# Kernel tuning notes

Measured on AMD Instinct MI355X. Metric: run time of the kernel, lower is better.

## Reference

```python
import jax, jax.numpy as jnp
import numpy as np

N_NODES = 100000
N_EDGES = 1600000
D_IN, D_HID, D_OUT = 128, 128, 40


def _sgconv(feat, W, b, src, dst, n_nodes):
    # DGL SGConv, k=1, norm='both': D^{-1/2} A D^{-1/2} X W + b
    ones = jnp.ones(dst.shape, dtype=feat.dtype)
    deg = jax.ops.segment_sum(ones, dst, num_segments=n_nodes)  # in-degrees
    norm = jnp.clip(deg, 1.0) ** -0.5  # [N]
    h = feat * norm[:, None]
    # sparse aggregation: gather from src, scatter-add to dst
    h = jax.ops.segment_sum(h[src], dst, num_segments=n_nodes)  # [N, d]
    h = h * norm[:, None]
    return h @ W + b


def setup_inputs() -> dict:
    key = jax.random.key(0)
    ks = jax.random.split(key, 6)
    features = jax.random.normal(ks[0], (N_NODES, D_IN), dtype=jnp.float32)
    src = jax.random.randint(ks[1], (N_EDGES,), 0, N_NODES, dtype=jnp.int32)
    dst = jax.random.randint(ks[2], (N_EDGES,), 0, N_NODES, dtype=jnp.int32)
    # Xavier-uniform init like DGL's fc
    lim1 = float(np.sqrt(6.0 / (D_IN + D_HID)))
    lim2 = float(np.sqrt(6.0 / (D_HID + D_OUT)))
    W1 = jax.random.uniform(ks[3], (D_IN, D_HID), jnp.float32, -lim1, lim1)
    b1 = jnp.zeros((D_HID,), dtype=jnp.float32)
    W2 = jax.random.uniform(ks[4], (D_HID, D_OUT), jnp.float32, -lim2, lim2)
    b2 = jnp.zeros((D_OUT,), dtype=jnp.float32)
    return {"features": features, "src": src, "dst": dst,
            "W1": W1, "b1": b1, "W2": W2, "b2": b2, "n_nodes": N_NODES}


def reference(features, src, dst, W1, b1, W2, b2, n_nodes):
    x = _sgconv(features, W1, b1, src, dst, n_nodes)
    x = jax.nn.elu(x)
    x = _sgconv(x, W2, b2, src, dst, n_nodes)
    return x
```

## Files before the change

kernel.cpp:

```cpp
#include <hip/hip_runtime.h>
#include <hip/hip_fp16.h>
#include <math.h>


#define DIN  128
#define DHID 128
#define DOUT 40
#define BSHIFT 9
#define BNODES 512

union U8  { uint2 u; __half2 h[2]; };
union U16 { uint4 u; __half2 h[4]; };

typedef _Float16     f16x8 __attribute__((ext_vector_type(8)));
typedef float        f32x4 __attribute__((ext_vector_type(4)));
union F16X8 { uint4 u; f16x8 f; };
union HCV   { __half h; unsigned short s; };
union FV4   { float4 h; f32x4 v; };

__device__ __forceinline__ float elu_f(float x) {
    return x > 0.0f ? x : (expf(x) - 1.0f);
}

__global__ void prep_pass1(const float* __restrict__ W1, const float* __restrict__ W2,
                           __half* __restrict__ w1f, __half* __restrict__ w2f,
                           const int* __restrict__ src, const int* __restrict__ dst,
                           int E, int NB, int cap,
                           int* __restrict__ bcur, int* __restrict__ bbuf) {
    __shared__ int cnt[256];
    __shared__ int wcur[256];
    if (blockIdx.x < 11) {
        int tid = blockIdx.x * 256 + threadIdx.x;
        if (tid < 2048) {
            int l = tid & 63;
            int t = (tid >> 6) & 3;
            int c = tid >> 8;
            int kb = t * 32 + (l >> 4) * 8, col = c * 16 + (l & 15);
            #pragma unroll
            for (int j = 0; j < 8; ++j)
                w1f[tid * 8 + j] = __float2half_rn(W1[(kb + j) * DHID + col]);
        } else if (tid < 2048 + 768) {
            int id = tid - 2048;
            int l = id & 63;
            int t = (id >> 6) & 3;
            int c = id >> 8;
            int kb = t * 32 + (l >> 4) * 8, col = c * 16 + (l & 15);
            #pragma unroll
            for (int j = 0; j < 8; ++j)
                w2f[id * 8 + j] = (col < DOUT) ? __float2half_rn(W2[(kb + j) * DOUT + col])
                                               : __float2half_rn(0.f);
        }
        return;
    }
    int bid = blockIdx.x - 11;
    int nblk = gridDim.x - 11;
    const int CHUNK = 8192;
    for (long base = (long)bid * CHUNK; base < E; base += (long)nblk * CHUNK) {
        int n = min(CHUNK, (int)(E - base));
        if (threadIdx.x < 256) cnt[threadIdx.x] = 0;
        __syncthreads();
        for (int i = threadIdx.x; i < n; i += blockDim.x) {
            int b = dst[base + i] >> BSHIFT;
            atomicAdd(&cnt[b], 1);
        }
        __syncthreads();
        if (threadIdx.x < NB) {
            int c = cnt[threadIdx.x];
            wcur[threadIdx.x] = (c > 0) ? atomicAdd(&bcur[threadIdx.x], c) : 0;
        }
        __syncthreads();
        for (int i = threadIdx.x; i < n; i += blockDim.x) {
            int s = src[base + i];
            int d = dst[base + i];
            int b = d >> BSHIFT;
            int slot = atomicAdd(&wcur[b], 1);
            if (slot < cap) bbuf[(long)b * cap + slot] = (s << BSHIFT) | (d & (BNODES - 1));
        }
        __syncthreads();
    }
}

__global__ void pass2_sort(const int* __restrict__ bbuf, const int* __restrict__ bcur,
                           int N, int NB, int cap,
                           float* __restrict__ norm, int* __restrict__ rowptr,
                           int* __restrict__ esrc) {
    __shared__ int cnt[BNODES];
    __shared__ int scnt[256];
    __shared__ int sgbase;
    int tid = threadIdx.x;
    int b = blockIdx.x;
    scnt[tid] = (tid < NB) ? bcur[tid] : 0;
    __syncthreads();
    if (tid == 0) {
        int run = 0;
        for (int i = 0; i < NB; ++i) { if (i == b) sgbase = run; run += scnt[i]; }
        if (b == NB - 1) rowptr[N] = run;
    }
    __syncthreads();
    int gbase = sgbase;
    int n_b = min(bcur[b], cap);
    int dbase = b << BSHIFT;
    const int* eb = bbuf + (long)b * cap;
    for (int i = tid; i < BNODES; i += blockDim.x) cnt[i] = 0;
    __syncthreads();
    for (int i = tid; i < n_b; i += blockDim.x)
        atomicAdd(&cnt[eb[i] & (BNODES - 1)], 1);
    __syncthreads();
    for (int i = tid; i < BNODES; i += blockDim.x) {
        int d = dbase + i;
        if (d < N) norm[d] = rsqrtf(fmaxf((float)cnt[i], 1.0f));
    }
    __syncthreads();
    if (tid == 0) {
        int run = 0;
        #pragma unroll 4
        for (int i = 0; i < BNODES; ++i) { int c = cnt[i]; cnt[i] = run; run += c; }
    }
    __syncthreads();
    for (int i = tid; i < BNODES; i += blockDim.x) {
        int d = dbase + i;
        if (d < N) rowptr[d] = gbase + cnt[i];
    }
    __syncthreads();
    for (int i = tid; i < n_b; i += blockDim.x) {
        int v = eb[i];
        int slot = atomicAdd(&cnt[v & (BNODES - 1)], 1);
        esrc[gbase + slot] = ((unsigned)v) >> BSHIFT;
    }
}

__global__ void perm_yconv(const int* __restrict__ rowptr, int* __restrict__ perm,
                           const float* __restrict__ feat, const float* __restrict__ norm,
                           __half* __restrict__ y, int N, int npermblk) {
    __shared__ int lcnt[1024];
    __shared__ int lbase[1024];
    if ((int)blockIdx.x < npermblk) {
        const int CHUNK = 4096;
        for (long base = (long)blockIdx.x * CHUNK; base < N; base += (long)npermblk * CHUNK) {
            int n = min(CHUNK, (int)(N - base));
            for (int i = threadIdx.x; i < 1024; i += 256) lcnt[i] = 0;
            __syncthreads();
            for (int i = threadIdx.x; i < n; i += 256) {
                int d = min(rowptr[base + i + 1] - rowptr[base + i], 1023);
                atomicAdd(&lcnt[d], 1);
            }
            __syncthreads();
            if (threadIdx.x == 0) {
                int run = 0;
                for (int i = 0; i < 1024; ++i) { int c = lcnt[i]; lbase[i] = run; run += c; }
            }
            __syncthreads();
            for (int i = threadIdx.x; i < 1024; i += 256) lcnt[i] = 0;
            __syncthreads();
            for (int i = threadIdx.x; i < n; i += 256) {
                int d = min(rowptr[base + i + 1] - rowptr[base + i], 1023);
                int pos = lbase[d] + atomicAdd(&lcnt[d], 1);
                perm[base + pos] = base + (int)i;
            }
            __syncthreads();
        }
        return;
    }
    long total = (long)N * 32;
    long stride = (long)(gridDim.x - npermblk) * 256;
    const float4* f4 = reinterpret_cast<const float4*>(feat);
    uint2* y2 = reinterpret_cast<uint2*>(y);
    for (long i = (long)(blockIdx.x - npermblk) * 256 + threadIdx.x; i < total; i += stride) {
        int n = (int)(i >> 5);
        float nm = norm[n];
        float4 v = f4[i];
        U8 o;
        o.h[0] = __floats2half2_rn(v.x * nm, v.y * nm);
        o.h[1] = __floats2half2_rn(v.z * nm, v.w * nm);
        y2[i] = o.u;
    }
}

__global__ void norm_from_deg(const int* __restrict__ deg, float* __restrict__ norm, int N) {
    int stride = gridDim.x * blockDim.x;
    for (int i = blockIdx.x * blockDim.x + threadIdx.x; i < N; i += stride)
        norm[i] = rsqrtf(fmaxf((float)deg[i], 1.0f));
}

__global__ void degi_kernel(const int* __restrict__ dst, int E, int* __restrict__ deg) {
    int stride = gridDim.x * blockDim.x;
    for (int i = blockIdx.x * blockDim.x + threadIdx.x; i < E; i += stride)
        atomicAdd(&deg[dst[i]], 1);
}


__global__ void gather1_kernel(const __half* __restrict__ y, const int* __restrict__ rowptr,
                               const int* __restrict__ esrc, const int* __restrict__ perm,
                               const float* __restrict__ norm,
                               __half* __restrict__ aggh, int N) {
    int lane = threadIdx.x & 15;
    long g = ((long)blockIdx.x * blockDim.x + threadIdx.x) >> 4;
    long gstride = ((long)gridDim.x * blockDim.x) >> 4;
    const uint4* y4 = reinterpret_cast<const uint4*>(y);
    uint4* a4 = reinterpret_cast<uint4*>(aggh);
    for (long gi = g; gi < N; gi += gstride) {
        int n = perm[gi];
        int beg = rowptr[n], end = rowptr[n + 1];
        float a0 = 0.f, a1 = 0.f, a2 = 0.f, a3 = 0.f;
        float a4f = 0.f, a5 = 0.f, a6 = 0.f, a7 = 0.f;
        int j = beg;
        for (; j + 1 < end; j += 2) {
            int s0 = esrc[j], s1 = esrc[j + 1];
            U16 u0, u1;
            u0.u = y4[(long)s0 * 16 + lane];
            u1.u = y4[(long)s1 * 16 + lane];
            float2 p0 = __half22float2(u0.h[0]), p1 = __half22float2(u0.h[1]);
            float2 p2 = __half22float2(u0.h[2]), p3 = __half22float2(u0.h[3]);
            float2 q0 = __half22float2(u1.h[0]), q1 = __half22float2(u1.h[1]);
            float2 q2 = __half22float2(u1.h[2]), q3 = __half22float2(u1.h[3]);
            a0 += p0.x + q0.x; a1 += p0.y + q0.y;
            a2 += p1.x + q1.x; a3 += p1.y + q1.y;
            a4f += p2.x + q2.x; a5 += p2.y + q2.y;
            a6 += p3.x + q3.x; a7 += p3.y + q3.y;
        }
        if (j < end) {
            int s0 = esrc[j];
            U16 u0; u0.u = y4[(long)s0 * 16 + lane];
            float2 p0 = __half22float2(u0.h[0]), p1 = __half22float2(u0.h[1]);
            float2 p2 = __half22float2(u0.h[2]), p3 = __half22float2(u0.h[3]);
            a0 += p0.x; a1 += p0.y; a2 += p1.x; a3 += p1.y;
            a4f += p2.x; a5 += p2.y; a6 += p3.x; a7 += p3.y;
        }
        float nm = norm[n];
        U16 o;
        o.h[0] = __floats2half2_rn(a0 * nm, a1 * nm);
        o.h[1] = __floats2half2_rn(a2 * nm, a3 * nm);
        o.h[2] = __floats2half2_rn(a4f * nm, a5 * nm);
        o.h[3] = __floats2half2_rn(a6 * nm, a7 * nm);
        a4[(long)n * 16 + lane] = o.u;
    }
}

__global__ void gather2_kernel(const __half* __restrict__ z, const int* __restrict__ rowptr,
                               const int* __restrict__ esrc, const int* __restrict__ perm,
                               const float* __restrict__ norm, const float* __restrict__ b2,
                               float* __restrict__ out, int N) {
    int lane = threadIdx.x & 63;
    int grp = lane / 5;
    int seg = lane - grp * 5;
    bool act = grp < 12;
    long wglob = ((long)blockIdx.x * blockDim.x + threadIdx.x) >> 6;
    long g0 = wglob * 12 + grp;
    long gstride = (((long)gridDim.x * blockDim.x) >> 6) * 12;
    const uint4* z4 = reinterpret_cast<const uint4*>(z);
    for (long gi = g0; gi < N; gi += gstride) {
        if (act) {
            int n = perm[gi];
            int beg = rowptr[n], end = rowptr[n + 1];
            float a0 = 0.f, a1 = 0.f, a2 = 0.f, a3 = 0.f;
            float a4f = 0.f, a5 = 0.f, a6 = 0.f, a7 = 0.f;
            int j = beg;
            for (; j + 1 < end; j += 2) {
                int s0 = esrc[j], s1 = esrc[j + 1];
                U16 u0, u1;
                u0.u = z4[(long)s0 * 5 + seg];
                u1.u = z4[(long)s1 * 5 + seg];
                float2 p0 = __half22float2(u0.h[0]), p1 = __half22float2(u0.h[1]);
                float2 p2 = __half22float2(u0.h[2]), p3 = __half22float2(u0.h[3]);
                float2 q0 = __half22float2(u1.h[0]), q1 = __half22float2(u1.h[1]);
                float2 q2 = __half22float2(u1.h[2]), q3 = __half22float2(u1.h[3]);
                a0 += p0.x + q0.x; a1 += p0.y + q0.y;
                a2 += p1.x + q1.x; a3 += p1.y + q1.y;
                a4f += p2.x + q2.x; a5 += p2.y + q2.y;
                a6 += p3.x + q3.x; a7 += p3.y + q3.y;
            }
            if (j < end) {
                int s0 = esrc[j];
                U16 u0; u0.u = z4[(long)s0 * 5 + seg];
                float2 p0 = __half22float2(u0.h[0]), p1 = __half22float2(u0.h[1]);
                float2 p2 = __half22float2(u0.h[2]), p3 = __half22float2(u0.h[3]);
                a0 += p0.x; a1 += p0.y; a2 += p1.x; a3 += p1.y;
                a4f += p2.x; a5 += p2.y; a6 += p3.x; a7 += p3.y;
            }
            float nm = norm[n];
            const float4* b4 = reinterpret_cast<const float4*>(b2);
            float4 bb0 = b4[seg * 2], bb1 = b4[seg * 2 + 1];
            FV4 o0, o1;
            o0.h.x = fmaf(a0, nm, bb0.x); o0.h.y = fmaf(a1, nm, bb0.y);
            o0.h.z = fmaf(a2, nm, bb0.z); o0.h.w = fmaf(a3, nm, bb0.w);
            o1.h.x = fmaf(a4f, nm, bb1.x); o1.h.y = fmaf(a5, nm, bb1.y);
            o1.h.z = fmaf(a6, nm, bb1.z); o1.h.w = fmaf(a7, nm, bb1.w);
            f32x4* out4 = reinterpret_cast<f32x4*>(out);
            __builtin_nontemporal_store(o0.v, &out4[(long)n * 10 + seg * 2]);
            __builtin_nontemporal_store(o1.v, &out4[(long)n * 10 + seg * 2 + 1]);
        }
    }
}


__launch_bounds__(256, 2)
__global__ void mmfused_kernel(const __half* __restrict__ aggh,
                               const __half* __restrict__ w1f, const __half* __restrict__ w2f,
                               const float* __restrict__ b1, const float* __restrict__ norm,
                               __half* __restrict__ z, int N) {
    __shared__ uint4 w1l[2048];
    __shared__ uint4 w2l[768];
    __shared__ unsigned short hl[64 * 128];
    int tid = threadIdx.x;
    const uint4* w1g = reinterpret_cast<const uint4*>(w1f);
    const uint4* w2g = reinterpret_cast<const uint4*>(w2f);
    for (int i = tid; i < 2048; i += 256) w1l[i] = w1g[i];
    for (int i = tid; i < 768; i += 256) w2l[i] = w2g[i];
    __syncthreads();

    int w = tid >> 6, l = tid & 63;
    int lr = l & 15, lg = l >> 4;
    float b1v[8];
    #pragma unroll
    for (int c = 0; c < 8; ++c) b1v[c] = b1[c * 16 + lr];

    int ntiles = (N + 63) >> 6;
    const uint4* ag = reinterpret_cast<const uint4*>(aggh);
    for (int tile = blockIdx.x; tile < ntiles; tile += gridDim.x) {
        int rb = tile << 6;
        int arow = rb + w * 16 + lr;
        int arc = min(arow, N - 1);
        F16X8 af[4];
        #pragma unroll
        for (int t = 0; t < 4; ++t) af[t].u = ag[(long)arc * 16 + t * 4 + lg];
        #pragma unroll
        for (int c = 0; c < 8; ++c) {
            f32x4 acc = {b1v[c], b1v[c], b1v[c], b1v[c]};
            #pragma unroll
            for (int t = 0; t < 4; ++t) {
                F16X8 bf; bf.u = w1l[(c * 4 + t) * 64 + l];
                acc = __builtin_amdgcn_mfma_f32_16x16x32_f16(af[t].f, bf.f, acc, 0, 0, 0);
            }
            int colb2 = (c * 16 + lr) * 2;
            #pragma unroll
            for (int i = 0; i < 4; ++i) {
                int rl = w * 16 + lg * 4 + i;
                HCV cv; cv.h = __float2half_rn(elu_f(acc[i]));
                int ba = (rl * 256 + colb2) ^ ((rl & 7) << 4);
                *reinterpret_cast<unsigned short*>(reinterpret_cast<char*>(hl) + ba) = cv.s;
            }
        }
        int rl2 = w * 16 + lr;
        int sw = (rl2 & 7) << 4;
        F16X8 hf[4];
        #pragma unroll
        for (int t = 0; t < 4; ++t) {
            int ba = (rl2 * 256 + (t * 32 + lg * 8) * 2) ^ sw;
            hf[t].u = *reinterpret_cast<const uint4*>(reinterpret_cast<const char*>(hl) + ba);
        }
        float nmv[4];
        #pragma unroll
        for (int i = 0; i < 4; ++i) {
            int r = rb + w * 16 + lg * 4 + i;
            nmv[i] = norm[min(r, N - 1)];
        }
        #pragma unroll
        for (int c = 0; c < 3; ++c) {
            f32x4 acc = {0.f, 0.f, 0.f, 0.f};
            #pragma unroll
            for (int t = 0; t < 4; ++t) {
                F16X8 bf; bf.u = w2l[(c * 4 + t) * 64 + l];
                acc = __builtin_amdgcn_mfma_f32_16x16x32_f16(hf[t].f, bf.f, acc, 0, 0, 0);
            }
            int col = c * 16 + lr;
            if (col < DOUT) {
                #pragma unroll
                for (int i = 0; i < 4; ++i) {
                    int r = rb + w * 16 + lg * 4 + i;
                    if (r < N) z[(long)r * DOUT + col] = __float2half_rn(acc[i] * nmv[i]);
                }
            }
        }
    }
}


__global__ void scatter1_kernel(const float* __restrict__ feat, const int* __restrict__ src,
                                const int* __restrict__ dst, const float* __restrict__ norm,
                                float* __restrict__ agg, int E) {
    long T = (long)blockIdx.x * blockDim.x + threadIdx.x;
    int l4 = (int)(T & 31);
    long e = T >> 5;
    long estride = ((long)gridDim.x * blockDim.x) >> 5;
    for (; e < E; e += estride) {
        int s = src[e], d = dst[e];
        float ns = norm[s];
        float4 v = reinterpret_cast<const float4*>(feat)[(long)s * 32 + l4];
        float* o = agg + (long)d * DIN + l4 * 4;
        atomicAdd(o + 0, v.x * ns);
        atomicAdd(o + 1, v.y * ns);
        atomicAdd(o + 2, v.z * ns);
        atomicAdd(o + 3, v.w * ns);
    }
}

__global__ void scatter2_kernel(const float* __restrict__ z, const int* __restrict__ src,
                                const int* __restrict__ dst, float* __restrict__ out, int E) {
    long T = (long)blockIdx.x * blockDim.x + threadIdx.x;
    int l = (int)(T & 15);
    long e = T >> 4;
    long estride = ((long)gridDim.x * blockDim.x) >> 4;
    for (; e < E; e += estride) {
        if (l < 10) {
            int s = src[e], d = dst[e];
            float4 v = reinterpret_cast<const float4*>(z)[(long)s * 10 + l];
            float* o = out + (long)d * DOUT + l * 4;
            atomicAdd(o + 0, v.x);
            atomicAdd(o + 1, v.y);
            atomicAdd(o + 2, v.z);
            atomicAdd(o + 3, v.w);
        }
    }
}

__launch_bounds__(256, 2)
__global__ void mm1f_kernel(float* __restrict__ xh, const float* __restrict__ W1,
                            const float* __restrict__ b1, const float* __restrict__ norm,
                            int N) {
    __shared__ float Wl[DIN * DHID];
    __shared__ float Xl[32 * DIN];
    for (int i = threadIdx.x; i < DIN * DHID; i += 256) Wl[i] = W1[i];
    int cg = threadIdx.x & 31;
    int rg = threadIdx.x >> 5;
    int c0 = cg * 4;
    for (long r0 = (long)blockIdx.x * 32; r0 < N; r0 += (long)gridDim.x * 32) {
        __syncthreads();
        for (int i = threadIdx.x; i < 32 * 32; i += 256) {
            int rr = i >> 5;
            long row = r0 + rr;
            float4 v = make_float4(0.f, 0.f, 0.f, 0.f);
            if (row < N) {
                v = reinterpret_cast<const float4*>(xh)[row * 32 + (i & 31)];
                float nm = norm[row];
                v.x *= nm; v.y *= nm; v.z *= nm; v.w *= nm;
            }
            reinterpret_cast<float4*>(Xl)[i] = v;
        }
        __syncthreads();
        float acc[4][4];
        float bx = b1[c0], by = b1[c0 + 1], bz = b1[c0 + 2], bw = b1[c0 + 3];
        #pragma unroll
        for (int r = 0; r < 4; ++r) { acc[r][0] = bx; acc[r][1] = by; acc[r][2] = bz; acc[r][3] = bw; }
        for (int k = 0; k < DIN; k += 4) {
            float4 w0 = *reinterpret_cast<const float4*>(&Wl[(k + 0) * DHID + c0]);
            float4 w1 = *reinterpret_cast<const float4*>(&Wl[(k + 1) * DHID + c0]);
            float4 w2 = *reinterpret_cast<const float4*>(&Wl[(k + 2) * DHID + c0]);
            float4 w3 = *reinterpret_cast<const float4*>(&Wl[(k + 3) * DHID + c0]);
            #pragma unroll
            for (int r = 0; r < 4; ++r) {
                float4 x = *reinterpret_cast<const float4*>(&Xl[(rg * 4 + r) * DIN + k]);
                acc[r][0] = fmaf(x.x, w0.x, fmaf(x.y, w1.x, fmaf(x.z, w2.x, fmaf(x.w, w3.x, acc[r][0]))));
                acc[r][1] = fmaf(x.x, w0.y, fmaf(x.y, w1.y, fmaf(x.z, w2.y, fmaf(x.w, w3.y, acc[r][1]))));
                acc[r][2] = fmaf(x.x, w0.z, fmaf(x.y, w1.z, fmaf(x.z, w2.z, fmaf(x.w, w3.z, acc[r][2]))));
                acc[r][3] = fmaf(x.x, w0.w, fmaf(x.y, w1.w, fmaf(x.z, w2.w, fmaf(x.w, w3.w, acc[r][3]))));
            }
        }
        #pragma unroll
        for (int r = 0; r < 4; ++r) {
            long row = r0 + rg * 4 + r;
            if (row < N) {
                float4 o;
                o.x = elu_f(acc[r][0]); o.y = elu_f(acc[r][1]);
                o.z = elu_f(acc[r][2]); o.w = elu_f(acc[r][3]);
                *reinterpret_cast<float4*>(&xh[row * DIN + c0]) = o;
            }
        }
    }
}

__launch_bounds__(256, 2)
__global__ void mm2f_kernel(const float* __restrict__ h, const float* __restrict__ W2,
                            const float* __restrict__ norm, float* __restrict__ z, int N) {
    __shared__ float Wl[DHID * DOUT];
    __shared__ float Xl[64 * DIN];
    for (int i = threadIdx.x; i < DHID * DOUT; i += 256) Wl[i] = W2[i];
    int cg = threadIdx.x & 15;
    int rg = threadIdx.x >> 4;
    int c0 = cg * 4;
    for (long r0 = (long)blockIdx.x * 64; r0 < N; r0 += (long)gridDim.x * 64) {
        __syncthreads();
        for (int i = threadIdx.x; i < 64 * 32; i += 256) {
            int rr = i >> 5;
            long row = r0 + rr;
            float4 v = make_float4(0.f, 0.f, 0.f, 0.f);
            if (row < N) v = reinterpret_cast<const float4*>(h)[row * 32 + (i & 31)];
            reinterpret_cast<float4*>(Xl)[i] = v;
        }
        __syncthreads();
        if (c0 < DOUT) {
            float acc[4][4];
            #pragma unroll
            for (int r = 0; r < 4; ++r) { acc[r][0] = 0.f; acc[r][1] = 0.f; acc[r][2] = 0.f; acc[r][3] = 0.f; }
            for (int k = 0; k < DHID; k += 4) {
                float4 w0 = *reinterpret_cast<const float4*>(&Wl[(k + 0) * DOUT + c0]);
                float4 w1 = *reinterpret_cast<const float4*>(&Wl[(k + 1) * DOUT + c0]);
                float4 w2 = *reinterpret_cast<const float4*>(&Wl[(k + 2) * DOUT + c0]);
                float4 w3 = *reinterpret_cast<const float4*>(&Wl[(k + 3) * DOUT + c0]);
                #pragma unroll
                for (int r = 0; r < 4; ++r) {
                    float4 x = *reinterpret_cast<const float4*>(&Xl[(rg * 4 + r) * DIN + k]);
                    acc[r][0] = fmaf(x.x, w0.x, fmaf(x.y, w1.x, fmaf(x.z, w2.x, fmaf(x.w, w3.x, acc[r][0]))));
                    acc[r][1] = fmaf(x.x, w0.y, fmaf(x.y, w1.y, fmaf(x.z, w2.y, fmaf(x.w, w3.y, acc[r][1]))));
                    acc[r][2] = fmaf(x.x, w0.z, fmaf(x.y, w1.z, fmaf(x.z, w2.z, fmaf(x.w, w3.z, acc[r][2]))));
                    acc[r][3] = fmaf(x.x, w0.w, fmaf(x.y, w1.w, fmaf(x.z, w2.w, fmaf(x.w, w3.w, acc[r][3]))));
                }
            }
            #pragma unroll
            for (int r = 0; r < 4; ++r) {
                long row = r0 + rg * 4 + r;
                if (row < N) {
                    float nm = norm[row];
                    float4 o;
                    o.x = acc[r][0] * nm; o.y = acc[r][1] * nm;
                    o.z = acc[r][2] * nm; o.w = acc[r][3] * nm;
                    *reinterpret_cast<float4*>(&z[row * DOUT + c0]) = o;
                }
            }
        }
    }
}

__global__ void final_kernel(float* __restrict__ out, const float* __restrict__ norm,
                             const float* __restrict__ b2, int N) {
    long total = (long)N * DOUT;
    long stride = (long)gridDim.x * blockDim.x;
    for (long i = (long)blockIdx.x * blockDim.x + threadIdx.x; i < total; i += stride) {
        int n = (int)(i / DOUT), d = (int)(i % DOUT);
        out[i] = fmaf(out[i], norm[n], b2[d]);
    }
}


static inline size_t al4k(size_t x) { return (x + 4095) & ~(size_t)4095; }

extern "C" void kernel_launch(void* const* d_in, const int* in_sizes, int n_in,
                              void* d_out, int out_size, void* d_ws, size_t ws_size,
                              hipStream_t stream) {
    const float* feat = (const float*)d_in[0];
    const int*   src  = (const int*)d_in[1];
    const int*   dst  = (const int*)d_in[2];
    const float* W1   = (const float*)d_in[3];
    const float* b1   = (const float*)d_in[4];
    const float* W2   = (const float*)d_in[5];
    const float* b2   = (const float*)d_in[6];
    int N = in_sizes[0] / DIN;
    int E = in_sizes[1];
    float* out = (float*)d_out;
    char* ws = (char*)d_ws;

    int NB = (N + BNODES - 1) >> BSHIFT;
    int cap = ((E / (NB > 0 ? NB : 1)) * 5 / 4 + 256 + 1) & ~1;

    size_t o_norm   = 0;
    size_t o_rowptr = o_norm   + al4k((size_t)N * 4);
    size_t o_bcur   = o_rowptr + al4k(((size_t)N + 1) * 4);
    size_t o_perm   = o_bcur   + al4k((size_t)(NB + 1) * 4);
    size_t o_esrc   = o_perm   + al4k((size_t)N * 4);
    size_t o_aggh   = o_esrc   + al4k((size_t)E * 4);
    size_t o_y      = o_aggh   + al4k((size_t)N * DIN * 2);
    size_t o_z      = o_y      + al4k((size_t)N * DIN * 2);
    size_t o_w1f    = o_z      + al4k((size_t)N * DOUT * 2);
    size_t o_w2f    = o_w1f    + al4k((size_t)16384 * 2);
    size_t need     = o_w2f    + al4k((size_t)6144 * 2);

    bool bb_fits = (size_t)NB * cap * 4 <= (size_t)N * DIN * 2;
    bool packs   = N <= (1 << 22);

    if (ws_size >= need && NB <= 256 && bb_fits && packs) {
        float*  norm   = (float*)(ws + o_norm);
        int*    rowptr = (int*)(ws + o_rowptr);
        int*    bcur   = (int*)(ws + o_bcur);
        int*    perm   = (int*)(ws + o_perm);
        int*    esrc   = (int*)(ws + o_esrc);
        __half* aggh   = (__half*)(ws + o_aggh);
        int*    bbuf   = (int*)(ws + o_aggh);
        __half* y      = (__half*)(ws + o_y);
        __half* z      = (__half*)(ws + o_z);
        __half* w1f    = (__half*)(ws + o_w1f);
        __half* w2f    = (__half*)(ws + o_w2f);

        hipMemsetAsync(bcur, 0, (size_t)(NB + 1) * 4, stream);

        int p1grid = (E + 8191) / 8192;
        prep_pass1<<<p1grid + 11, 256, 0, stream>>>(W1, W2, w1f, w2f, src, dst, E, NB, cap, bcur, bbuf);
        pass2_sort<<<NB, 256, 0, stream>>>(bbuf, bcur, N, NB, cap, norm, rowptr, esrc);
        int npermblk = (N + 4095) / 4096;
        perm_yconv<<<npermblk + 2048, 256, 0, stream>>>(rowptr, perm, feat, norm, y, N, npermblk);

        gather1_kernel<<<(N * 16 + 255) / 256, 256, 0, stream>>>(y, rowptr, esrc, perm, norm, aggh, N);
        mmfused_kernel<<<512, 256, 0, stream>>>(aggh, w1f, w2f, b1, norm, z, N);
        gather2_kernel<<<(N + 47) / 48, 256, 0, stream>>>(z, rowptr, esrc, perm, norm, b2, out, N);
    } else {
        size_t f_norm = 0;
        size_t f_agg  = f_norm + al4k((size_t)N * 4);
        size_t f_z    = f_agg  + al4k((size_t)N * DIN * 4);
        float* norm = (float*)(ws + f_norm);
        float* agg  = (float*)(ws + f_agg);
        float* z    = (float*)(ws + f_z);
        int*   degi = (int*)(ws + f_norm);

        hipMemsetAsync(degi, 0, (size_t)N * 4, stream);
        hipMemsetAsync(agg, 0, (size_t)N * DIN * 4, stream);
        hipMemsetAsync(d_out, 0, (size_t)N * DOUT * 4, stream);

        degi_kernel<<<1024, 256, 0, stream>>>(dst, E, degi);
        norm_from_deg<<<(N + 255) / 256, 256, 0, stream>>>(degi, (float*)degi, N);
        scatter1_kernel<<<4096, 256, 0, stream>>>(feat, src, dst, norm, agg, E);
        mm1f_kernel<<<(N + 31) / 32, 256, 0, stream>>>(agg, W1, b1, norm, N);
        mm2f_kernel<<<(N + 63) / 64, 256, 0, stream>>>(agg, W2, norm, z, N);
        scatter2_kernel<<<4096, 256, 0, stream>>>(z, src, dst, out, E);
        final_kernel<<<4096, 256, 0, stream>>>(out, norm, b2, N);
    }
}
```

Baseline: 232.0 us.

## Fuse first-layer gather with both MFMA matmuls, drop aggh buffer

Merges the layer-1 neighbor gather with the W1 matmul, ELU and W2 matmul into one kernel that processes 16 nodes per block through swizzled LDS tiles. This removes the fp16 aggregate round trip to global memory and one kernel launch. The bucket buffer now aliases the y region, and the pass-1 chunk size is shrunk to 2048 to launch more blocks. The trade-off is that each block reads weights from global or L2 instead of caching them in LDS, and per-block MFMA work is small relative to the gather.

```diff
diff --git a/kernel.cpp b/kernel.cpp
--- a/kernel.cpp
+++ b/kernel.cpp
@@ -54,7 +54,7 @@
     }
     int bid = blockIdx.x - 11;
     int nblk = gridDim.x - 11;
-    const int CHUNK = 8192;
+    const int CHUNK = 2048;
     for (long base = (long)bid * CHUNK; base < E; base += (long)nblk * CHUNK) {
         int n = min(CHUNK, (int)(E - base));
         if (threadIdx.x < 256) cnt[threadIdx.x] = 0;
@@ -188,51 +188,116 @@
         atomicAdd(&deg[dst[i]], 1);
 }
 
-
-__global__ void gather1_kernel(const __half* __restrict__ y, const int* __restrict__ rowptr,
-                               const int* __restrict__ esrc, const int* __restrict__ perm,
-                               const float* __restrict__ norm,
-                               __half* __restrict__ aggh, int N) {
-    int lane = threadIdx.x & 15;
-    long g = ((long)blockIdx.x * blockDim.x + threadIdx.x) >> 4;
-    long gstride = ((long)gridDim.x * blockDim.x) >> 4;
+__launch_bounds__(256, 5)
+__global__ void gather1mm_kernel(const __half* __restrict__ y, const int* __restrict__ rowptr,
+                                 const int* __restrict__ esrc, const int* __restrict__ perm,
+                                 const float* __restrict__ norm,
+                                 const __half* __restrict__ w1f, const __half* __restrict__ w2f,
+                                 const float* __restrict__ b1, __half* __restrict__ z, int N) {
+    __shared__ unsigned short Xt[16 * 128];
+    __shared__ unsigned short Ht[16 * 128];
+    __shared__ int   tN[16];
+    __shared__ float tNm[16];
+    int tid = threadIdx.x;
+    int g = tid >> 4, l16 = tid & 15;
+
+    long gi = (long)blockIdx.x * 16 + g;
+    int n = -1, beg = 0, end = 0;
+    float nm = 0.f;
+    if (gi < N) { n = perm[gi]; beg = rowptr[n]; end = rowptr[n + 1]; nm = norm[n]; }
+
+    float a0 = 0.f, a1 = 0.f, a2 = 0.f, a3 = 0.f;
+    float a4f = 0.f, a5 = 0.f, a6 = 0.f, a7 = 0.f;
     const uint4* y4 = reinterpret_cast<const uint4*>(y);
-    uint4* a4 = reinterpret_cast<uint4*>(aggh);
-    for (long gi = g; gi < N; gi += gstride) {
-        int n = perm[gi];
-        int beg = rowptr[n], end = rowptr[n + 1];
-        float a0 = 0.f, a1 = 0.f, a2 = 0.f, a3 = 0.f;
-        float a4f = 0.f, a5 = 0.f, a6 = 0.f, a7 = 0.f;
-        int j = beg;
-        for (; j + 1 < end; j += 2) {
-            int s0 = esrc[j], s1 = esrc[j + 1];
-            U16 u0, u1;
-            u0.u = y4[(long)s0 * 16 + lane];
-            u1.u = y4[(long)s1 * 16 + lane];
-            float2 p0 = __half22float2(u0.h[0]), p1 = __half22float2(u0.h[1]);
-            float2 p2 = __half22float2(u0.h[2]), p3 = __half22float2(u0.h[3]);
-            float2 q0 = __half22float2(u1.h[0]), q1 = __half22float2(u1.h[1]);
-            float2 q2 = __half22float2(u1.h[2]), q3 = __half22float2(u1.h[3]);
-            a0 += p0.x + q0.x; a1 += p0.y + q0.y;
-            a2 += p1.x + q1.x; a3 += p1.y + q1.y;
-            a4f += p2.x + q2.x; a5 += p2.y + q2.y;
-            a6 += p3.x + q3.x; a7 += p3.y + q3.y;
-        }
-        if (j < end) {
-            int s0 = esrc[j];
-            U16 u0; u0.u = y4[(long)s0 * 16 + lane];
-            float2 p0 = __half22float2(u0.h[0]), p1 = __half22float2(u0.h[1]);
-            float2 p2 = __half22float2(u0.h[2]), p3 = __half22float2(u0.h[3]);
-            a0 += p0.x; a1 += p0.y; a2 += p1.x; a3 += p1.y;
-            a4f += p2.x; a5 += p2.y; a6 += p3.x; a7 += p3.y;
-        }
-        float nm = norm[n];
-        U16 o;
-        o.h[0] = __floats2half2_rn(a0 * nm, a1 * nm);
-        o.h[1] = __floats2half2_rn(a2 * nm, a3 * nm);
-        o.h[2] = __floats2half2_rn(a4f * nm, a5 * nm);
-        o.h[3] = __floats2half2_rn(a6 * nm, a7 * nm);
-        a4[(long)n * 16 + lane] = o.u;
+    int j = beg;
+    for (; j + 1 < end; j += 2) {
+        int s0 = esrc[j], s1 = esrc[j + 1];
+        U16 u0, u1;
+        u0.u = y4[(long)s0 * 16 + l16];
+        u1.u = y4[(long)s1 * 16 + l16];
+        float2 p0 = __half22float2(u0.h[0]), p1 = __half22float2(u0.h[1]);
+        float2 p2 = __half22float2(u0.h[2]), p3 = __half22float2(u0.h[3]);
+        float2 q0 = __half22float2(u1.h[0]), q1 = __half22float2(u1.h[1]);
+        float2 q2 = __half22float2(u1.h[2]), q3 = __half22float2(u1.h[3]);
+        a0 += p0.x + q0.x; a1 += p0.y + q0.y;
+        a2 += p1.x + q1.x; a3 += p1.y + q1.y;
+        a4f += p2.x + q2.x; a5 += p2.y + q2.y;
+        a6 += p3.x + q3.x; a7 += p3.y + q3.y;
+    }
+    if (j < end) {
+        int s0 = esrc[j];
+        U16 u0; u0.u = y4[(long)s0 * 16 + l16];
+        float2 p0 = __half22float2(u0.h[0]), p1 = __half22float2(u0.h[1]);
+        float2 p2 = __half22float2(u0.h[2]), p3 = __half22float2(u0.h[3]);
+        a0 += p0.x; a1 += p0.y; a2 += p1.x; a3 += p1.y;
+        a4f += p2.x; a5 += p2.y; a6 += p3.x; a7 += p3.y;
+    }
+    U16 o;
+    o.h[0] = __floats2half2_rn(a0 * nm, a1 * nm);
+    o.h[1] = __floats2half2_rn(a2 * nm, a3 * nm);
+    o.h[2] = __floats2half2_rn(a4f * nm, a5 * nm);
+    o.h[3] = __floats2half2_rn(a6 * nm, a7 * nm);
+    {
+        int ba = (g * 256 + l16 * 16) ^ ((g & 7) << 4);
+        *reinterpret_cast<uint4*>(reinterpret_cast<char*>(Xt) + ba) = o.u;
+    }
+    if (l16 == 0) { tN[g] = n; tNm[g] = nm; }
+    __syncthreads();
+
+    int w = tid >> 6, l = tid & 63;
+    int lr = l & 15, lg = l >> 4;
+    F16X8 af[4];
+    #pragma unroll
+    for (int t = 0; t < 4; ++t) {
+        int ba = (lr * 256 + (t * 32 + lg * 8) * 2) ^ ((lr & 7) << 4);
+        af[t].u = *reinterpret_cast<const uint4*>(reinterpret_cast<const char*>(Xt) + ba);
+    }
+    const uint4* w1g = reinterpret_cast<const uint4*>(w1f);
+    const uint4* w2g = reinterpret_cast<const uint4*>(w2f);
+    #pragma unroll
+    for (int cc = 0; cc < 2; ++cc) {
+        int c = w * 2 + cc;
+        float bb = b1[c * 16 + lr];
+        f32x4 acc = {bb, bb, bb, bb};
+        #pragma unroll
+        for (int t = 0; t < 4; ++t) {
+            F16X8 bf; bf.u = w1g[(c * 4 + t) * 64 + l];
+            acc = __builtin_amdgcn_mfma_f32_16x16x32_f16(af[t].f, bf.f, acc, 0, 0, 0);
+        }
+        int colb2 = (c * 16 + lr) * 2;
+        #pragma unroll
+        for (int i = 0; i < 4; ++i) {
+            int rl = lg * 4 + i;
+            HCV cv; cv.h = __float2half_rn(elu_f(acc[i]));
+            int ba = (rl * 256 + colb2) ^ ((rl & 7) << 4);
+            *reinterpret_cast<unsigned short*>(reinterpret_cast<char*>(Ht) + ba) = cv.s;
+        }
+    }
+    __syncthreads();
+
+    if (w < 3) {
+        F16X8 hf[4];
+        #pragma unroll
+        for (int t = 0; t < 4; ++t) {
+            int ba = (lr * 256 + (t * 32 + lg * 8) * 2) ^ ((lr & 7) << 4);
+            hf[t].u = *reinterpret_cast<const uint4*>(reinterpret_cast<const char*>(Ht) + ba);
+        }
+        f32x4 acc = {0.f, 0.f, 0.f, 0.f};
+        #pragma unroll
+        for (int t = 0; t < 4; ++t) {
+            F16X8 bf; bf.u = w2g[(w * 4 + t) * 64 + l];
+            acc = __builtin_amdgcn_mfma_f32_16x16x32_f16(hf[t].f, bf.f, acc, 0, 0, 0);
+        }
+        int col = w * 16 + lr;
+        if (col < DOUT) {
+            #pragma unroll
+            for (int i = 0; i < 4; ++i) {
+                int rl = lg * 4 + i;
+                int nn = tN[rl];
+                if (nn >= 0)
+                    z[(long)nn * DOUT + col] = __float2half_rn(acc[i] * tNm[rl]);
+            }
+        }
     }
 }
 
@@ -293,88 +358,6 @@
 }
 
 
-__launch_bounds__(256, 2)
-__global__ void mmfused_kernel(const __half* __restrict__ aggh,
-                               const __half* __restrict__ w1f, const __half* __restrict__ w2f,
-                               const float* __restrict__ b1, const float* __restrict__ norm,
-                               __half* __restrict__ z, int N) {
-    __shared__ uint4 w1l[2048];
-    __shared__ uint4 w2l[768];
-    __shared__ unsigned short hl[64 * 128];
-    int tid = threadIdx.x;
-    const uint4* w1g = reinterpret_cast<const uint4*>(w1f);
-    const uint4* w2g = reinterpret_cast<const uint4*>(w2f);
-    for (int i = tid; i < 2048; i += 256) w1l[i] = w1g[i];
-    for (int i = tid; i < 768; i += 256) w2l[i] = w2g[i];
-    __syncthreads();
-
-    int w = tid >> 6, l = tid & 63;
-    int lr = l & 15, lg = l >> 4;
-    float b1v[8];
-    #pragma unroll
-    for (int c = 0; c < 8; ++c) b1v[c] = b1[c * 16 + lr];
-
-    int ntiles = (N + 63) >> 6;
-    const uint4* ag = reinterpret_cast<const uint4*>(aggh);
-    for (int tile = blockIdx.x; tile < ntiles; tile += gridDim.x) {
-        int rb = tile << 6;
-        int arow = rb + w * 16 + lr;
-        int arc = min(arow, N - 1);
-        F16X8 af[4];
-        #pragma unroll
-        for (int t = 0; t < 4; ++t) af[t].u = ag[(long)arc * 16 + t * 4 + lg];
-        #pragma unroll
-        for (int c = 0; c < 8; ++c) {
-            f32x4 acc = {b1v[c], b1v[c], b1v[c], b1v[c]};
-            #pragma unroll
-            for (int t = 0; t < 4; ++t) {
-                F16X8 bf; bf.u = w1l[(c * 4 + t) * 64 + l];
-                acc = __builtin_amdgcn_mfma_f32_16x16x32_f16(af[t].f, bf.f, acc, 0, 0, 0);
-            }
-            int colb2 = (c * 16 + lr) * 2;
-            #pragma unroll
-            for (int i = 0; i < 4; ++i) {
-                int rl = w * 16 + lg * 4 + i;
-                HCV cv; cv.h = __float2half_rn(elu_f(acc[i]));
-                int ba = (rl * 256 + colb2) ^ ((rl & 7) << 4);
-                *reinterpret_cast<unsigned short*>(reinterpret_cast<char*>(hl) + ba) = cv.s;
-            }
-        }
-        int rl2 = w * 16 + lr;
-        int sw = (rl2 & 7) << 4;
-        F16X8 hf[4];
-        #pragma unroll
-        for (int t = 0; t < 4; ++t) {
-            int ba = (rl2 * 256 + (t * 32 + lg * 8) * 2) ^ sw;
-            hf[t].u = *reinterpret_cast<const uint4*>(reinterpret_cast<const char*>(hl) + ba);
-        }
-        float nmv[4];
-        #pragma unroll
-        for (int i = 0; i < 4; ++i) {
-            int r = rb + w * 16 + lg * 4 + i;
-            nmv[i] = norm[min(r, N - 1)];
-        }
-        #pragma unroll
-        for (int c = 0; c < 3; ++c) {
-            f32x4 acc = {0.f, 0.f, 0.f, 0.f};
-            #pragma unroll
-            for (int t = 0; t < 4; ++t) {
-                F16X8 bf; bf.u = w2l[(c * 4 + t) * 64 + l];
-                acc = __builtin_amdgcn_mfma_f32_16x16x32_f16(hf[t].f, bf.f, acc, 0, 0, 0);
-            }
-            int col = c * 16 + lr;
-            if (col < DOUT) {
-                #pragma unroll
-                for (int i = 0; i < 4; ++i) {
-                    int r = rb + w * 16 + lg * 4 + i;
-                    if (r < N) z[(long)r * DOUT + col] = __float2half_rn(acc[i] * nmv[i]);
-                }
-            }
-        }
-    }
-}
-
-
 __global__ void scatter1_kernel(const float* __restrict__ feat, const int* __restrict__ src,
                                 const int* __restrict__ dst, const float* __restrict__ norm,
                                 float* __restrict__ agg, int E) {
@@ -556,8 +539,7 @@
     size_t o_bcur   = o_rowptr + al4k(((size_t)N + 1) * 4);
     size_t o_perm   = o_bcur   + al4k((size_t)(NB + 1) * 4);
     size_t o_esrc   = o_perm   + al4k((size_t)N * 4);
-    size_t o_aggh   = o_esrc   + al4k((size_t)E * 4);
-    size_t o_y      = o_aggh   + al4k((size_t)N * DIN * 2);
+    size_t o_y      = o_esrc   + al4k((size_t)E * 4);
     size_t o_z      = o_y      + al4k((size_t)N * DIN * 2);
     size_t o_w1f    = o_z      + al4k((size_t)N * DOUT * 2);
     size_t o_w2f    = o_w1f    + al4k((size_t)16384 * 2);
@@ -572,23 +554,22 @@
         int*    bcur   = (int*)(ws + o_bcur);
         int*    perm   = (int*)(ws + o_perm);
         int*    esrc   = (int*)(ws + o_esrc);
-        __half* aggh   = (__half*)(ws + o_aggh);
-        int*    bbuf   = (int*)(ws + o_aggh);
         __half* y      = (__half*)(ws + o_y);
+        int*    bbuf   = (int*)(ws + o_y);
         __half* z      = (__half*)(ws + o_z);
         __half* w1f    = (__half*)(ws + o_w1f);
         __half* w2f    = (__half*)(ws + o_w2f);
 
         hipMemsetAsync(bcur, 0, (size_t)(NB + 1) * 4, stream);
 
-        int p1grid = (E + 8191) / 8192;
+        int p1grid = (E + 2047) / 2048;
         prep_pass1<<<p1grid + 11, 256, 0, stream>>>(W1, W2, w1f, w2f, src, dst, E, NB, cap, bcur, bbuf);
         pass2_sort<<<NB, 256, 0, stream>>>(bbuf, bcur, N, NB, cap, norm, rowptr, esrc);
         int npermblk = (N + 4095) / 4096;
         perm_yconv<<<npermblk + 2048, 256, 0, stream>>>(rowptr, perm, feat, norm, y, N, npermblk);
 
-        gather1_kernel<<<(N * 16 + 255) / 256, 256, 0, stream>>>(y, rowptr, esrc, perm, norm, aggh, N);
-        mmfused_kernel<<<512, 256, 0, stream>>>(aggh, w1f, w2f, b1, norm, z, N);
+        gather1mm_kernel<<<(N + 15) / 16, 256, 0, stream>>>(y, rowptr, esrc, perm, norm,
+                                                            w1f, w2f, b1, z, N);
         gather2_kernel<<<(N + 47) / 48, 256, 0, stream>>>(z, rowptr, esrc, perm, norm, b2, out, N);
     } else {
         size_t f_norm = 0;
```

After: 210.6 us. 9.2% less time.
